# Kernel optimization log

Hardware: AMD Instinct MI355X
Metric: run time of the kernel (lower is better)

Reference implementation:

```python
import jax, jax.numpy as jnp
import numpy as np

INPUT_DIM = 1024
HIDDEN_DIM = 2048
LATENT_DIM = 256
NUM_EMBEDDINGS = 8192
COMMITMENT_COST = 0.25
BATCH = 16384


def setup_inputs() -> dict:
    key = jax.random.key(0)
    ks = jax.random.split(key, 10)
    def lin(k, fan_in, fan_out):
        # torch nn.Linear default init: U(-1/sqrt(fan_in), 1/sqrt(fan_in))
        bound = 1.0 / np.sqrt(fan_in)
        kw, kb = jax.random.split(k)
        W = jax.random.uniform(kw, (fan_in, fan_out), jnp.float32, -bound, bound)
        b = jax.random.uniform(kb, (fan_out,), jnp.float32, -bound, bound)
        return W, b
    enc_w1, enc_b1 = lin(ks[0], INPUT_DIM, HIDDEN_DIM)
    enc_w2, enc_b2 = lin(ks[1], HIDDEN_DIM, LATENT_DIM)
    dec_w1, dec_b1 = lin(ks[2], LATENT_DIM, HIDDEN_DIM)
    dec_w2, dec_b2 = lin(ks[3], HIDDEN_DIM, INPUT_DIM)
    # codebook init: U(-1/K, 1/K)
    codebook = jax.random.uniform(ks[4], (NUM_EMBEDDINGS, LATENT_DIM), jnp.float32,
                                  -1.0 / NUM_EMBEDDINGS, 1.0 / NUM_EMBEDDINGS)
    x = jax.random.uniform(ks[5], (BATCH, INPUT_DIM), jnp.float32)
    return {"x": x,
            "enc_w1": enc_w1, "enc_b1": enc_b1, "enc_w2": enc_w2, "enc_b2": enc_b2,
            "codebook": codebook,
            "dec_w1": dec_w1, "dec_b1": dec_b1, "dec_w2": dec_w2, "dec_b2": dec_b2}


def reference(x, enc_w1, enc_b1, enc_w2, enc_b2, codebook,
              dec_w1, dec_b1, dec_w2, dec_b2):
    # Encoder: relu(x W1 + b1) W2 + b2 -> z [N, latent]
    h = jax.nn.relu(x @ enc_w1 + enc_b1)
    z = h @ enc_w2 + enc_b2

    # Vector quantizer: squared-L2 distances to codebook [N, K]
    d = (jnp.sum(z * z, axis=1, keepdims=True)
         + jnp.sum(codebook * codebook, axis=1)
         - 2.0 * (z @ codebook.T))
    idx = jnp.argmin(d, axis=1)          # [N] int
    z_q = codebook[idx]                   # gather [N, latent]

    vq_loss = jnp.mean((jax.lax.stop_gradient(z_q) - z) ** 2)
    commit_loss = COMMITMENT_COST * jnp.mean((z_q - jax.lax.stop_gradient(z)) ** 2)
    loss = vq_loss + commit_loss

    # straight-through estimator
    z_q = z + jax.lax.stop_gradient(z_q - z)

    # Decoder: sigmoid(relu(z_q Wd1 + bd1) Wd2 + bd2)
    hd = jax.nn.relu(z_q @ dec_w1 + dec_b1)
    x_recon = jax.nn.sigmoid(hd @ dec_w2 + dec_b2)
    return (x_recon, loss)
```

## Files before the change

kernel.cpp:

```cpp
#include <hip/hip_runtime.h>
#include <math.h>

typedef unsigned short u16;
typedef __bf16 bf16x8 __attribute__((ext_vector_type(8)));
typedef float  f32x4  __attribute__((ext_vector_type(4)));

constexpr int B_  = 16384;
constexpr int DIN = 1024;
constexpr int DH  = 2048;
constexpr int DL  = 256;
constexpr int NE  = 8192;

__device__ __forceinline__ u16 f2bf(float f) {
    union { float f; unsigned u; } v; v.f = f;
    unsigned r = v.u + 0x7fffu + ((v.u >> 16) & 1u);
    return (u16)(r >> 16);
}
__device__ __forceinline__ float bf2f(u16 h) {
    union { unsigned u; float f; } v; v.u = ((unsigned)h) << 16;
    return v.f;
}

#define GLD16(gp, lp)                                                  \
    __builtin_amdgcn_global_load_lds(                                  \
        (__attribute__((address_space(1))) void*)(gp),                 \
        (__attribute__((address_space(3))) void*)(lp), 16, 0, 0)

__global__ __launch_bounds__(256)
void cast_bf16(const float* __restrict__ in, u16* __restrict__ out)
{
    const size_t i = ((size_t)blockIdx.x * 256 + threadIdx.x) * 4;
    float4 v = *(const float4*)(in + i);
    ushort4 o;
    o.x = f2bf(v.x); o.y = f2bf(v.y); o.z = f2bf(v.z); o.w = f2bf(v.w);
    *(ushort4*)(out + i) = o;
}

__global__ __launch_bounds__(256)
void transpose_cast(const float* __restrict__ in, u16* __restrict__ out,
                    int R, int C)
{
    __shared__ float t[32][33];
    const int tx = threadIdx.x & 31, ty = threadIdx.x >> 5;
    const long bx = blockIdx.x;
    const long by = blockIdx.y;
#pragma unroll
    for (int p = 0; p < 4; ++p)
        t[ty + p * 8][tx] = in[(by * 32 + ty + p * 8) * (long)C + bx * 32 + tx];
    __syncthreads();
#pragma unroll
    for (int p = 0; p < 4; ++p)
        out[(bx * 32 + ty + p * 8) * (long)R + by * 32 + tx] = f2bf(t[tx][ty + p * 8]);
}

__global__ __launch_bounds__(256)
void cn2_kernel(const float* __restrict__ cb, float* __restrict__ cn2)
{
    const int code = (blockIdx.x * 256 + threadIdx.x) >> 6;
    const int lane = threadIdx.x & 63;
    float4 v = *(const float4*)(cb + (long)code * DL + lane * 4);
    float s = fmaf(v.x, v.x, fmaf(v.y, v.y, fmaf(v.z, v.z, v.w * v.w)));
#pragma unroll
    for (int off = 32; off; off >>= 1) s += __shfl_down(s, off);
    if (lane == 0) cn2[code] = 0.5f * s;
}

template <int EPI>
__global__ __launch_bounds__(512, 4)
void gemm_big_bf16(const u16* __restrict__ A, const u16* __restrict__ Bt,
                   const float* __restrict__ bias, void* __restrict__ Cout,
                   int M, int N, int K)
{
    __shared__ __align__(16) u16 As[2][256 * 32];
    __shared__ __align__(16) u16 Bs[2][128 * 32];

    const int tid = threadIdx.x;
    const int w = tid >> 6, l = tid & 63;
    const int wm = w >> 1, wn = w & 1;

    const int nbx   = N >> 7;
    const int nwg   = (M >> 8) * nbx;
    const int chunk = nwg >> 3;
    const int wg    = ((int)blockIdx.x & 7) * chunk + ((int)blockIdx.x >> 3);
    const long by   = wg / nbx;
    const long bx   = wg % nbx;

    const int lr  = l >> 2;
    const int lsw = (l & 3) ^ (lr & 3);
    const int lg  = l >> 4, lm = l & 15;
    const int rch = (0 ^ (lm & 3));

    const u16* Abase = A  + (size_t)(by * 256) * K;
    const u16* Bbase = Bt + (size_t)(bx * 128) * K;

    f32x4 acc[4][4] = {};

    auto stage = [&](int k0, int b) {
        u16* dA = &As[b][0];
        u16* dB = &Bs[b][0];
#pragma unroll
        for (int i = 0; i < 2; ++i) {
            const int seg = w * 2 + i;
            GLD16(Abase + (size_t)(seg * 16 + lr) * K + k0 + lsw * 8,
                  dA + seg * 512);
        }
        GLD16(Bbase + (size_t)(w * 16 + lr) * K + k0 + lsw * 8,
              dB + w * 512);
    };

    const int NT = K >> 5;
    stage(0, 0);
    __syncthreads();

    const int sx = lm & 3;
    for (int t = 0; t < NT; ++t) {
        if (t + 1 < NT) stage((t + 1) << 5, (t + 1) & 1);

        const u16* as = &As[t & 1][0];
        const u16* bs = &Bs[t & 1][0];
        bf16x8 af[4], bfr[4];
#pragma unroll
        for (int m = 0; m < 4; ++m) {
            const int R = wm * 64 + m * 16 + lm;
            af[m] = *(const bf16x8*)&as[R * 32 + ((lg ^ sx) * 8)];
        }
#pragma unroll
        for (int n = 0; n < 4; ++n) {
            const int R = wn * 64 + n * 16 + lm;
            bfr[n] = *(const bf16x8*)&bs[R * 32 + ((lg ^ sx) * 8)];
        }
#pragma unroll
        for (int m = 0; m < 4; ++m)
#pragma unroll
            for (int n = 0; n < 4; ++n)
                acc[m][n] = __builtin_amdgcn_mfma_f32_16x16x32_bf16(
                    af[m], bfr[n], acc[m][n], 0, 0, 0);
        __syncthreads();
    }

#pragma unroll
    for (int n = 0; n < 4; ++n) {
        const long col = bx * 128 + wn * 64 + n * 16 + lm;
        const float bb = bias[col];
#pragma unroll
        for (int m = 0; m < 4; ++m) {
#pragma unroll
            for (int j = 0; j < 4; ++j) {
                const long row = by * 256 + wm * 64 + m * 16 + lg * 4 + j;
                float e = acc[m][n][j] + bb;
                if (EPI == 1) e = fmaxf(e, 0.f);
                if (EPI == 2) {
                    e = 1.f / (1.f + expf(-e));
                    ((float*)Cout)[row * (long)N + col] = e;
                } else {
                    ((u16*)Cout)[row * (long)N + col] = f2bf(e);
                }
            }
        }
    }
}

template <int EPI>
__global__ __launch_bounds__(256)
void gemm_bt_bf16(const u16* __restrict__ A, const u16* __restrict__ Bt,
                  const float* __restrict__ bias, void* __restrict__ Cout,
                  int M, int N, int K)
{
    __shared__ __align__(16) u16 As[2 * 4096];
    __shared__ __align__(16) u16 Bs[2 * 4096];

    const int tid = threadIdx.x;
    const int w = tid >> 6, l = tid & 63;
    const int wr = w >> 1, wc = w & 1;

    const int nbx   = N >> 7;
    const int nwg   = (M >> 7) * nbx;
    const int chunk = nwg >> 3;
    const int wg    = ((int)blockIdx.x & 7) * chunk + ((int)blockIdx.x >> 3);
    const long by   = wg / nbx;
    const long bx   = wg % nbx;

    const int lr = l >> 2;
    const int lc = (l & 3) * 8;
    const int lg = l >> 4, lm = l & 15;

    const u16* Abase = A  + (size_t)(by * 128) * K;
    const u16* Bbase = Bt + (size_t)(bx * 128) * K;

    f32x4 acc[4][4] = {};

    auto stage = [&](int k0, int b) {
        u16* dA = As + b * 4096;
        u16* dB = Bs + b * 4096;
#pragma unroll
        for (int i = 0; i < 2; ++i) {
            const int seg = w * 2 + i;
            GLD16(Abase + (size_t)(seg * 16 + lr) * K + k0 + lc, dA + seg * 512);
            GLD16(Bbase + (size_t)(seg * 16 + lr) * K + k0 + lc, dB + seg * 512);
        }
    };

    const int NT = K >> 5;
    stage(0, 0);
    __syncthreads();

    for (int t = 0; t < NT; ++t) {
        if (t + 1 < NT) stage((t + 1) << 5, (t + 1) & 1);

        const u16* as = As + (t & 1) * 4096;
        const u16* bs = Bs + (t & 1) * 4096;
        bf16x8 af[4], bfr[4];
#pragma unroll
        for (int m = 0; m < 4; ++m)
            af[m] = *(const bf16x8*)&as[(wr * 64 + m * 16 + lm) * 32 + lg * 8];
#pragma unroll
        for (int n = 0; n < 4; ++n)
            bfr[n] = *(const bf16x8*)&bs[(wc * 64 + n * 16 + lm) * 32 + lg * 8];
#pragma unroll
        for (int m = 0; m < 4; ++m)
#pragma unroll
            for (int n = 0; n < 4; ++n)
                acc[m][n] = __builtin_amdgcn_mfma_f32_16x16x32_bf16(
                    af[m], bfr[n], acc[m][n], 0, 0, 0);
        __syncthreads();
    }

#pragma unroll
    for (int n = 0; n < 4; ++n) {
        const long col = bx * 128 + wc * 64 + n * 16 + lm;
        const float bb = bias[col];
#pragma unroll
        for (int m = 0; m < 4; ++m) {
#pragma unroll
            for (int j = 0; j < 4; ++j) {
                const long row = by * 128 + wr * 64 + m * 16 + lg * 4 + j;
                float e = acc[m][n][j] + bb;
                if (EPI == 1) e = fmaxf(e, 0.f);
                if (EPI == 2) {
                    e = 1.f / (1.f + expf(-e));
                    ((float*)Cout)[row * (long)N + col] = e;
                } else {
                    ((u16*)Cout)[row * (long)N + col] = f2bf(e);
                }
            }
        }
    }
}

__global__ __launch_bounds__(256, 2)
void vq_score2(const u16* __restrict__ z, const u16* __restrict__ cbt,
               const float* __restrict__ cn2,
               float* __restrict__ val8, int* __restrict__ idx8)
{
    __shared__ __align__(16) u16 lds[32768];

    const int tid = threadIdx.x;
    const int w = tid >> 6, l = tid & 63;
    const int rq = blockIdx.x >> 3;
    const int q  = blockIdx.x & 7;

    const int st_row8 = tid >> 5;
    const int st_s    = (tid & 31) ^ st_row8;
    const int lg = l >> 4, lm = l & 15;
    const int swz_x = l & 7;

    bf16x8 af[4][8];
    const long zbase_row = (long)rq * 256;
#pragma unroll
    for (int h = 0; h < 2; ++h) {
#pragma unroll
        for (int i = 0; i < 16; ++i) {
            const int row = i * 8 + st_row8;
            const u16* g = z + (zbase_row + h * 128 + row) * DL + st_s * 8;
            GLD16(g, lds + ((size_t)i * 256 + w * 64) * 8);
        }
        __syncthreads();
        if ((w >> 1) == h) {
            const int lrow0 = (w & 1) * 64;
#pragma unroll
            for (int m = 0; m < 4; ++m) {
                const int lrow = lrow0 + m * 16 + lm;
#pragma unroll
                for (int kg = 0; kg < 8; ++kg) {
                    const int s = (kg * 4 + lg) ^ swz_x;
                    af[m][kg] = *(const bf16x8*)&lds[lrow * 256 + s * 8];
                }
            }
        }
        __syncthreads();
    }

    const int code00 = q * (NE / 8);

    float bestv[16];
    int   besti[16];
#pragma unroll
    for (int k = 0; k < 16; ++k) { bestv[k] = 1e30f; besti[k] = 0; }

    auto stage_tile = [&](int t) {
        const int b = t & 1;
#pragma unroll
        for (int i = 0; i < 8; ++i) {
            const int c = i * 8 + st_row8;
            const u16* g = cbt + (size_t)(code00 + t * 64 + c) * DL + st_s * 8;
            GLD16(g, lds + ((size_t)b * 16384 + ((size_t)i * 256 + w * 64) * 8));
        }
    };

    stage_tile(0);
    __syncthreads();

    for (int t = 0; t < 16; ++t) {
        if (t < 15) stage_tile(t + 1);
        const u16* buf = lds + (size_t)(t & 1) * 16384;

#pragma unroll
        for (int n = 0; n < 4; ++n) {
            const int code_g = code00 + t * 64 + n * 16 + lm;
            const float cn2v = cn2[code_g];
            bf16x8 bfr[8];
#pragma unroll
            for (int kg = 0; kg < 8; ++kg) {
                const int lrow = n * 16 + lm;
                const int s = (kg * 4 + lg) ^ swz_x;
                bfr[kg] = *(const bf16x8*)&buf[lrow * 256 + s * 8];
            }
            f32x4 acc[4] = {};
#pragma unroll
            for (int kg = 0; kg < 8; ++kg)
#pragma unroll
                for (int m = 0; m < 4; ++m)
                    acc[m] = __builtin_amdgcn_mfma_f32_16x16x32_bf16(
                        af[m][kg], bfr[kg], acc[m], 0, 0, 0);
#pragma unroll
            for (int m = 0; m < 4; ++m)
#pragma unroll
                for (int j = 0; j < 4; ++j) {
                    const float s = cn2v - acc[m][j];
                    const int k16 = m * 4 + j;
                    if (s < bestv[k16]) { bestv[k16] = s; besti[k16] = code_g; }
                }
        }
        __syncthreads();
    }

#pragma unroll
    for (int off = 1; off < 16; off <<= 1) {
#pragma unroll
        for (int k = 0; k < 16; ++k) {
            const float ov = __shfl_xor(bestv[k], off);
            const int   oi = __shfl_xor(besti[k], off);
            if (ov < bestv[k] || (ov == bestv[k] && oi < besti[k])) {
                bestv[k] = ov; besti[k] = oi;
            }
        }
    }
    if (lm == 0) {
#pragma unroll
        for (int m = 0; m < 4; ++m)
#pragma unroll
            for (int j = 0; j < 4; ++j) {
                const long row = zbase_row + w * 64 + m * 16 + lg * 4 + j;
                val8[(size_t)q * B_ + row] = bestv[m * 4 + j];
                idx8[(size_t)q * B_ + row] = besti[m * 4 + j];
            }
    }
}

__global__ __launch_bounds__(256)
void vq_select2(const float* __restrict__ val8, const int* __restrict__ idx8,
                const u16* __restrict__ z, const float* __restrict__ cb,
                u16* __restrict__ zq, float* __restrict__ partial)
{
    __shared__ int   s_idx[256];
    __shared__ float s_red[4];
    const int tid = threadIdx.x;
    const long row = (long)blockIdx.x * 256 + tid;

    float bv = val8[row];
    int   bi = idx8[row];
#pragma unroll
    for (int qq = 1; qq < 8; ++qq) {
        const float v = val8[(size_t)qq * B_ + row];
        const int   i = idx8[(size_t)qq * B_ + row];
        if (v < bv || (v == bv && i < bi)) { bv = v; bi = i; }
    }
    s_idx[tid] = bi;
    __syncthreads();

    float ls = 0.f;
    const int sub = tid & 7;
#pragma unroll
    for (int pass = 0; pass < 8; ++pass) {
        const int rl = pass * 32 + (tid >> 3);
        const int gi = s_idx[rl];
        const long rg = (long)blockIdx.x * 256 + rl;
#pragma unroll
        for (int tt = 0; tt < 8; ++tt) {
            const int d = sub * 4 + tt * 32;
            float4 c4 = *(const float4*)(cb + (long)gi * DL + d);
            ushort4 zu = *(const ushort4*)(z + rg * DL + d);
            ushort4 qo;
            qo.x = f2bf(c4.x); qo.y = f2bf(c4.y);
            qo.z = f2bf(c4.z); qo.w = f2bf(c4.w);
            *(ushort4*)(zq + rg * DL + d) = qo;
            const float dx = c4.x - bf2f(zu.x), dy = c4.y - bf2f(zu.y);
            const float dz = c4.z - bf2f(zu.z), dw = c4.w - bf2f(zu.w);
            ls += dx * dx + dy * dy + dz * dz + dw * dw;
        }
    }
#pragma unroll
    for (int off = 32; off; off >>= 1) ls += __shfl_down(ls, off);
    if ((tid & 63) == 0) s_red[tid >> 6] = ls;
    __syncthreads();
    if (tid == 0)
        partial[blockIdx.x] = s_red[0] + s_red[1] + s_red[2] + s_red[3];
}

__global__ __launch_bounds__(256)
void loss_finalize(const float* __restrict__ partial, float* __restrict__ out)
{
    __shared__ float s_red[4];
    const int tid = threadIdx.x;
    float s = (tid < 64) ? partial[tid] : 0.f;
#pragma unroll
    for (int off = 32; off; off >>= 1) s += __shfl_down(s, off);
    if ((tid & 63) == 0) s_red[tid >> 6] = s;
    __syncthreads();
    if (tid == 0)
        out[0] = 1.25f * (s_red[0] + s_red[1] + s_red[2] + s_red[3])
                 / (float)((long)B_ * DL);
}

extern "C" void kernel_launch(void* const* d_in, const int* in_sizes, int n_in,
                              void* d_out, int out_size, void* d_ws, size_t ws_size,
                              hipStream_t stream)
{
    const float* x   = (const float*)d_in[0];
    const float* ew1 = (const float*)d_in[1];
    const float* eb1 = (const float*)d_in[2];
    const float* ew2 = (const float*)d_in[3];
    const float* eb2 = (const float*)d_in[4];
    const float* cbk = (const float*)d_in[5];
    const float* dw1 = (const float*)d_in[6];
    const float* db1 = (const float*)d_in[7];
    const float* dw2 = (const float*)d_in[8];
    const float* db2 = (const float*)d_in[9];
    float* out = (float*)d_out;

    char* p = (char*)d_ws;
    auto alloc = [&](size_t bytes) {
        char* r = p; p += (bytes + 255) & ~(size_t)255; return r;
    };
    u16*   x_bf  = (u16*)alloc((size_t)B_ * DIN * 2);
    u16*   h_bf  = (u16*)alloc((size_t)B_ * DH * 2);
    u16*   z_bf  = (u16*)alloc((size_t)B_ * DL * 2);
    u16*   zq_bf = (u16*)alloc((size_t)B_ * DL * 2);
    u16*   cb_bf = (u16*)alloc((size_t)NE * DL * 2);
    u16*   w1t   = (u16*)alloc((size_t)DH * DIN * 2);
    u16*   w2t   = (u16*)alloc((size_t)DL * DH * 2);
    u16*   wd1t  = (u16*)alloc((size_t)DH * DL * 2);
    u16*   wd2t  = (u16*)alloc((size_t)DIN * DH * 2);
    float* cn2   = (float*)alloc((size_t)NE * 4);
    float* val8  = (float*)alloc((size_t)8 * B_ * 4);
    int*   idx8  = (int*)alloc((size_t)8 * B_ * 4);
    float* part  = (float*)alloc(64 * 4);

    cast_bf16<<<(size_t)B_ * DIN / 1024, 256, 0, stream>>>(x, x_bf);
    cast_bf16<<<(size_t)NE * DL / 1024, 256, 0, stream>>>(cbk, cb_bf);
    transpose_cast<<<dim3(DH / 32, DIN / 32), 256, 0, stream>>>(ew1, w1t, DIN, DH);
    transpose_cast<<<dim3(DL / 32, DH / 32), 256, 0, stream>>>(ew2, w2t, DH, DL);
    transpose_cast<<<dim3(DH / 32, DL / 32), 256, 0, stream>>>(dw1, wd1t, DL, DH);
    transpose_cast<<<dim3(DIN / 32, DH / 32), 256, 0, stream>>>(dw2, wd2t, DH, DIN);
    cn2_kernel<<<NE / 4, 256, 0, stream>>>(cbk, cn2);

    gemm_big_bf16<1><<<(B_ / 256) * (DH / 128), 512, 0, stream>>>(
        x_bf, w1t, eb1, h_bf, B_, DH, DIN);
    gemm_bt_bf16<0><<<(B_ / 128) * (DL / 128), 256, 0, stream>>>(
        h_bf, w2t, eb2, z_bf, B_, DL, DH);

    vq_score2<<<512, 256, 0, stream>>>(z_bf, cb_bf, cn2, val8, idx8);
    vq_select2<<<B_ / 256, 256, 0, stream>>>(val8, idx8, z_bf, cbk, zq_bf, part);
    loss_finalize<<<1, 256, 0, stream>>>(part, out + (size_t)B_ * DIN);

    gemm_big_bf16<1><<<(B_ / 256) * (DH / 128), 512, 0, stream>>>(
        zq_bf, wd1t, db1, h_bf, B_, DH, DL);
    gemm_big_bf16<2><<<(B_ / 256) * (DIN / 128), 512, 0, stream>>>(
        h_bf, wd2t, db2, out, B_, DIN, DH);
}
```

Measured before the change: 340.4 us.

## Triple-buffer GEMM LDS staging with vmcnt waits and new bank swizzle

```diff
diff --git a/kernel.cpp b/kernel.cpp
--- a/kernel.cpp
+++ b/kernel.cpp
@@ -26,6 +26,12 @@
         (__attribute__((address_space(1))) void*)(gp),                 \
         (__attribute__((address_space(3))) void*)(lp), 16, 0, 0)
 
+#define SCHED0() __builtin_amdgcn_sched_barrier(0)
+#define BARRIER() do { SCHED0(); __builtin_amdgcn_s_barrier(); SCHED0(); } while (0)
+#define WAITV0() asm volatile("s_waitcnt vmcnt(0)" ::: "memory")
+#define WAITV3() asm volatile("s_waitcnt vmcnt(3)" ::: "memory")
+#define WAITV4() asm volatile("s_waitcnt vmcnt(4)" ::: "memory")
+
 __global__ __launch_bounds__(256)
 void cast_bf16(const float* __restrict__ in, u16* __restrict__ out)
 {
@@ -71,8 +77,8 @@
                    const float* __restrict__ bias, void* __restrict__ Cout,
                    int M, int N, int K)
 {
-    __shared__ __align__(16) u16 As[2][256 * 32];
-    __shared__ __align__(16) u16 Bs[2][128 * 32];
+    __shared__ __align__(16) u16 As[3 * 8192];
+    __shared__ __align__(16) u16 Bs[3 * 4096];
 
     const int tid = threadIdx.x;
     const int w = tid >> 6, l = tid & 63;
@@ -86,9 +92,9 @@
     const long bx   = wg % nbx;
 
     const int lr  = l >> 2;
-    const int lsw = (l & 3) ^ (lr & 3);
+    const int lsw = (l & 3) ^ ((l >> 3) & 3);
     const int lg  = l >> 4, lm = l & 15;
-    const int rch = (0 ^ (lm & 3));
+    const int sx  = (lm >> 1) & 3;
 
     const u16* Abase = A  + (size_t)(by * 256) * K;
     const u16* Bbase = Bt + (size_t)(bx * 128) * K;
@@ -96,8 +102,8 @@
     f32x4 acc[4][4] = {};
 
     auto stage = [&](int k0, int b) {
-        u16* dA = &As[b][0];
-        u16* dB = &Bs[b][0];
+        u16* dA = As + b * 8192;
+        u16* dB = Bs + b * 4096;
 #pragma unroll
         for (int i = 0; i < 2; ++i) {
             const int seg = w * 2 + i;
@@ -110,14 +116,16 @@
 
     const int NT = K >> 5;
     stage(0, 0);
-    __syncthreads();
-
-    const int sx = lm & 3;
+    stage(32, 1);
+
+    int cur = 0, pre = 2;
     for (int t = 0; t < NT; ++t) {
-        if (t + 1 < NT) stage((t + 1) << 5, (t + 1) & 1);
-
-        const u16* as = &As[t & 1][0];
-        const u16* bs = &Bs[t & 1][0];
+        if (t + 1 < NT) { WAITV3(); } else { WAITV0(); }
+        BARRIER();
+        if (t + 2 < NT) stage((t + 2) << 5, pre);
+
+        const u16* as = As + cur * 8192;
+        const u16* bs = Bs + cur * 4096;
         bf16x8 af[4], bfr[4];
 #pragma unroll
         for (int m = 0; m < 4; ++m) {
@@ -135,7 +143,9 @@
             for (int n = 0; n < 4; ++n)
                 acc[m][n] = __builtin_amdgcn_mfma_f32_16x16x32_bf16(
                     af[m], bfr[n], acc[m][n], 0, 0, 0);
-        __syncthreads();
+
+        cur = (cur == 2) ? 0 : cur + 1;
+        pre = (pre == 2) ? 0 : pre + 1;
     }
 
 #pragma unroll
@@ -166,8 +176,8 @@
                   const float* __restrict__ bias, void* __restrict__ Cout,
                   int M, int N, int K)
 {
-    __shared__ __align__(16) u16 As[2 * 4096];
-    __shared__ __align__(16) u16 Bs[2 * 4096];
+    __shared__ __align__(16) u16 As[3 * 4096];
+    __shared__ __align__(16) u16 Bs[3 * 4096];
 
     const int tid = threadIdx.x;
     const int w = tid >> 6, l = tid & 63;
@@ -180,9 +190,10 @@
     const long by   = wg / nbx;
     const long bx   = wg % nbx;
 
-    const int lr = l >> 2;
-    const int lc = (l & 3) * 8;
-    const int lg = l >> 4, lm = l & 15;
+    const int lr  = l >> 2;
+    const int lsw = (l & 3) ^ ((l >> 3) & 3);
+    const int lg  = l >> 4, lm = l & 15;
+    const int sx  = (lm >> 1) & 3;
 
     const u16* Abase = A  + (size_t)(by * 128) * K;
     const u16* Bbase = Bt + (size_t)(bx * 128) * K;
@@ -195,34 +206,39 @@
 #pragma unroll
         for (int i = 0; i < 2; ++i) {
             const int seg = w * 2 + i;
-            GLD16(Abase + (size_t)(seg * 16 + lr) * K + k0 + lc, dA + seg * 512);
-            GLD16(Bbase + (size_t)(seg * 16 + lr) * K + k0 + lc, dB + seg * 512);
+            GLD16(Abase + (size_t)(seg * 16 + lr) * K + k0 + lsw * 8, dA + seg * 512);
+            GLD16(Bbase + (size_t)(seg * 16 + lr) * K + k0 + lsw * 8, dB + seg * 512);
         }
     };
 
     const int NT = K >> 5;
     stage(0, 0);
-    __syncthreads();
-
+    stage(32, 1);
+
+    int cur = 0, pre = 2;
     for (int t = 0; t < NT; ++t) {
-        if (t + 1 < NT) stage((t + 1) << 5, (t + 1) & 1);
-
-        const u16* as = As + (t & 1) * 4096;
-        const u16* bs = Bs + (t & 1) * 4096;
+        if (t + 1 < NT) { WAITV4(); } else { WAITV0(); }
+        BARRIER();
+        if (t + 2 < NT) stage((t + 2) << 5, pre);
+
+        const u16* as = As + cur * 4096;
+        const u16* bs = Bs + cur * 4096;
         bf16x8 af[4], bfr[4];
 #pragma unroll
         for (int m = 0; m < 4; ++m)
-            af[m] = *(const bf16x8*)&as[(wr * 64 + m * 16 + lm) * 32 + lg * 8];
+            af[m] = *(const bf16x8*)&as[(wr * 64 + m * 16 + lm) * 32 + ((lg ^ sx) * 8)];
 #pragma unroll
         for (int n = 0; n < 4; ++n)
-            bfr[n] = *(const bf16x8*)&bs[(wc * 64 + n * 16 + lm) * 32 + lg * 8];
+            bfr[n] = *(const bf16x8*)&bs[(wc * 64 + n * 16 + lm) * 32 + ((lg ^ sx) * 8)];
 #pragma unroll
         for (int m = 0; m < 4; ++m)
 #pragma unroll
             for (int n = 0; n < 4; ++n)
                 acc[m][n] = __builtin_amdgcn_mfma_f32_16x16x32_bf16(
                     af[m], bfr[n], acc[m][n], 0, 0, 0);
-        __syncthreads();
+
+        cur = (cur == 2) ? 0 : cur + 1;
+        pre = (pre == 2) ? 0 : pre + 1;
     }
 
 #pragma unroll
```

New measurement: 337.2 us. About the same (-0.9%).
